# Performance work log

Measured on AMD Instinct MI355X. Metric: run time of the kernel, lower is better.

## Reference

```python
import jax, jax.numpy as jnp
import numpy as np
import math

B, D, H, W, C = 1, 16, 56, 56, 256
WD, WH, WW = 2, 7, 7
NH, NP = 8, 4
N = WD * WH * WW          # 98 tokens per window
HD = C // NH
NWIN = (D // WD) * (H // WH) * (W // WW)  # 512


def layernorm(x, g, b, eps=1e-5):
    m = x.mean(-1, keepdims=True)
    v = jnp.mean((x - m) ** 2, -1, keepdims=True)
    return (x - m) * jax.lax.rsqrt(v + eps) * g + b


def _reference_points():
    zz = (jnp.arange(WD, dtype=jnp.float32) + 0.5) / WD
    yy = (jnp.arange(WH, dtype=jnp.float32) + 0.5) / WH
    xx = (jnp.arange(WW, dtype=jnp.float32) + 0.5) / WW
    gz, gy, gx = jnp.meshgrid(zz, yy, xx, indexing='ij')
    return jnp.stack([gx.ravel(), gy.ravel(), gz.ravel()], -1)  # (N, 3) in xyz order


def _trilinear(value, loc):
    # value: (Bn, N, NH, HD); loc: (Bn, N, NH, NP, 3) normalized xyz in [0,1]
    # grid_sample semantics: align_corners=False, zero padding
    Bn = value.shape[0]
    v = value.transpose(0, 2, 1, 3)  # (Bn, NH, S, HD), S == N (window volume)
    px = loc[..., 0] * WW - 0.5
    py = loc[..., 1] * WH - 0.5
    pz = loc[..., 2] * WD - 0.5
    x0, y0, z0 = jnp.floor(px), jnp.floor(py), jnp.floor(pz)
    out = jnp.zeros(loc.shape[:-1] + (HD,), value.dtype)
    for dz in (0, 1):
        for dy in (0, 1):
            for dx in (0, 1):
                xi, yi, zi = x0 + dx, y0 + dy, z0 + dz
                wgt = (1 - jnp.abs(px - xi)) * (1 - jnp.abs(py - yi)) * (1 - jnp.abs(pz - zi))
                valid = ((xi >= 0) & (xi < WW) & (yi >= 0) & (yi < WH) & (zi >= 0) & (zi < WD)).astype(value.dtype)
                idx = (jnp.clip(zi, 0, WD - 1) * (WH * WW) + jnp.clip(yi, 0, WH - 1) * WW
                       + jnp.clip(xi, 0, WW - 1)).astype(jnp.int32)  # (Bn, N, NH, NP)
                idxf = idx.transpose(0, 2, 1, 3).reshape(Bn, NH, N * NP)
                g = jnp.take_along_axis(v, idxf[..., None], axis=2)  # (Bn, NH, N*NP, HD)
                g = g.reshape(Bn, NH, N, NP, HD).transpose(0, 2, 1, 3, 4)
                out = out + g * (wgt * valid)[..., None]
    return out  # (Bn, N, NH, NP, HD)


def setup_inputs():
    key = jax.random.key(0)
    ks = jax.random.split(key, 12)

    def lin(k, fin, fout):
        s = 1.0 / np.sqrt(fin)
        kw, kb = jax.random.split(k)
        return (jax.random.uniform(kw, (fin, fout), jnp.float32, -s, s),
                jax.random.uniform(kb, (fout,), jnp.float32, -s, s))

    val_w, val_b = lin(ks[2], C, C)
    off_w, off_b = lin(ks[3], C, NH * NP * 3)
    aw_w, aw_b = lin(ks[4], C, NH * NP)
    out_w, out_b = lin(ks[5], C, C)
    proj_w, proj_b = lin(ks[6], C, C)
    fc1_w, fc1_b = lin(ks[7], C, 4 * C)
    fc2_w, fc2_b = lin(ks[8], 4 * C, C)
    return dict(
        x=jax.random.normal(ks[0], (B, D, H, W, C), jnp.float32),
        mask=jax.random.uniform(ks[1], (NWIN, N, WD, WH, WW), jnp.float32),
        norm1_g=jnp.ones((C,), jnp.float32), norm1_b=jnp.zeros((C,), jnp.float32),
        val_w=val_w, val_b=val_b, off_w=off_w, off_b=off_b,
        aw_w=aw_w, aw_b=aw_b, out_w=out_w, out_b=out_b,
        anorm_g=jnp.ones((C,), jnp.float32), anorm_b=jnp.zeros((C,), jnp.float32),
        proj_w=proj_w, proj_b=proj_b,
        norm2_g=jnp.ones((C,), jnp.float32), norm2_b=jnp.zeros((C,), jnp.float32),
        fc1_w=fc1_w, fc1_b=fc1_b, fc2_w=fc2_w, fc2_b=fc2_b)


def reference(x, mask, norm1_g, norm1_b, val_w, val_b, off_w, off_b, aw_w, aw_b,
              out_w, out_b, anorm_g, anorm_b, proj_w, proj_b,
              norm2_g, norm2_b, fc1_w, fc1_b, fc2_w, fc2_b):
    shortcut = x
    xn = layernorm(x, norm1_g, norm1_b)
    # window partition (dims divisible by window, shift_size = 0 -> no pad/roll)
    xw = xn.reshape(B, D // WD, WD, H // WH, WH, W // WW, WW, C)
    xw = xw.transpose(0, 1, 3, 5, 2, 4, 6, 7).reshape(-1, N, C)  # (B*NWIN, N, C)
    Bn = B * NWIN
    # --- PositionEmbeddingSine over the per-window mask ---
    z_e = jnp.cumsum(mask, 2) * mask / math.pi
    y_e = jnp.cumsum(mask, 3) * mask / math.pi
    x_e = jnp.cumsum(mask, 4) * mask / math.pi
    emb = mask * (jnp.sin(x_e) + jnp.sin(math.pi * y_e) + z_e)
    emb = emb.reshape(NWIN, N, N)  # flatten(2); N == WD*WH*WW
    diag = jnp.diagonal(emb, axis1=1, axis2=2)  # (NWIN, N)
    q = (xw.reshape(B, NWIN, N, C) + diag[None, :, :, None]).reshape(Bn, N, C)
    # --- MS3DDeformAttn over single level = window ---
    ref = _reference_points()  # (N, 3)
    value = (xw @ val_w + val_b).reshape(Bn, N, NH, HD)
    off = (q @ off_w + off_b).reshape(Bn, N, NH, NP, 3)
    aw = jax.nn.softmax((q @ aw_w + aw_b).reshape(Bn, N, NH, NP), axis=-1)
    loc = ref[None, :, None, None, :] + off / jnp.array([WW, WH, WD], jnp.float32)
    sampled = _trilinear(value, loc)                       # (Bn, N, NH, NP, HD)
    attn = (sampled * aw[..., None]).sum(3).reshape(Bn, N, C) @ out_w + out_b
    # WindowAttention3D epilogue: proj(norm(x + attn))
    xw = layernorm(xw + attn, anorm_g, anorm_b) @ proj_w + proj_b
    # window reverse
    xr = xw.reshape(B, D // WD, H // WH, W // WW, WD, WH, WW, C)
    xr = xr.transpose(0, 1, 4, 2, 5, 3, 6, 7).reshape(B, D, H, W, C)
    x = shortcut + xr
    # MLP branch
    h = layernorm(x, norm2_g, norm2_b)
    h = jax.nn.gelu(h @ fc1_w + fc1_b)
    return x + (h @ fc2_w + fc2_b)
```

## Files before the change

### kernel.cpp

```cpp
#include <hip/hip_runtime.h>
#include <hip/hip_bf16.h>
#include <hip/hip_fp16.h>

#define B2F(x) __bfloat162float(x)
#define F2B(x) __float2bfloat16(x)

typedef __bf16 bf16x8 __attribute__((ext_vector_type(8)));
typedef float floatx4 __attribute__((ext_vector_type(4)));

static constexpr int MROWS = 50176;
static constexpr int CDIM  = 256;
static constexpr int MCHUNK = 25088;

enum { MODE_BF16 = 0, MODE_VALOFFAW = 1, MODE_REVERSE = 3, MODE_GELU = 4, MODE_FC2 = 5, MODE_ATTN = 6 };

#if defined(__has_builtin)
#if __has_builtin(__builtin_amdgcn_global_load_lds)
#define HAS_GLL 1
#endif
#endif
#ifndef HAS_GLL
#define HAS_GLL 0
#endif


__device__ __forceinline__ void win_decode(int r, int& tok) {
    int w = r / 98, n = r - w * 98;
    int dB = w >> 6, hB = (w >> 3) & 7, wB = w & 7;
    int z = n / 49, n2 = n - z * 49, yy = n2 / 7, xx = n2 - yy * 7;
    tok = ((dB * 2 + z) * 56 + hB * 7 + yy) * 56 + wB * 7 + xx;
}

__device__ __forceinline__ float bf2f(unsigned short u) {
    return __uint_as_float(((unsigned)u) << 16);
}

__device__ __forceinline__ float wave_sum64(float v) {
#pragma unroll
    for (int off = 32; off > 0; off >>= 1) v += __shfl_xor(v, off, 64);
    return v;
}


__global__ __launch_bounds__(256) void fused_pre(
    const float* __restrict__ x, const float* __restrict__ n1g, const float* __restrict__ n1b,
    __hip_bfloat16* __restrict__ xw,
    const float* __restrict__ mask, float* __restrict__ diag, float* __restrict__ csum,
    const float* __restrict__ val_w, const float* __restrict__ off_w,
    const float* __restrict__ aw_w,  const float* __restrict__ out_w,
    const float* __restrict__ proj_w, const float* __restrict__ fc1_w,
    const float* __restrict__ fc2_w,
    __hip_bfloat16* __restrict__ valT, __hip_bfloat16* __restrict__ offawT,
    __hip_bfloat16* __restrict__ outT, __hip_bfloat16* __restrict__ projT,
    __hip_bfloat16* __restrict__ fc1T, __hip_bfloat16* __restrict__ fc2T) {
    const int bid = blockIdx.x;
    const int tid = threadIdx.x;

    if (bid < 2944) {
        const float* src; __hip_bfloat16* dst; int K, N, base;
        if (bid < 256)       { src = val_w;  dst = valT;            K = 256;  N = 256;  base = 0; }
        else if (bid < 352)  { src = off_w;  dst = offawT;          K = 256;  N = 96;   base = 256; }
        else if (bid < 384)  { src = aw_w;   dst = offawT + 96*256; K = 256;  N = 32;   base = 352; }
        else if (bid < 640)  { src = out_w;  dst = outT;            K = 256;  N = 256;  base = 384; }
        else if (bid < 896)  { src = proj_w; dst = projT;           K = 256;  N = 256;  base = 640; }
        else if (bid < 1920) { src = fc1_w;  dst = fc1T;            K = 256;  N = 1024; base = 896; }
        else                 { src = fc2_w;  dst = fc2T;            K = 1024; N = 256;  base = 1920; }
        int i = (bid - base) * 256 + tid;
        if (i >= K * N) return;
        int nn = i / K, kk = i - nn * K;
        dst[(size_t)nn * K + kk] = F2B(src[(size_t)kk * N + nn]);
    } else if (bid < 3140) {
        int r = (bid - 2944) * 256 + tid;
        int n = r % 98;
        int z = n / 49, n2 = n - z * 49, yy = n2 / 7, xx = n2 - yy * 7;
        const float* mb = mask + (size_t)r * 98;
        float m = mb[z * 49 + yy * 7 + xx];
        float sz = 0.f, sy = 0.f, sx = 0.f;
        for (int k = 0; k <= z; ++k)  sz += mb[k * 49 + yy * 7 + xx];
        for (int k = 0; k <= yy; ++k) sy += mb[z * 49 + k * 7 + xx];
        for (int k = 0; k <= xx; ++k) sx += mb[z * 49 + yy * 7 + k];
        const float PI = 3.14159265358979323846f;
        diag[r] = m * (sinf(sx * m / PI) + sinf(sy * m) + sz * m / PI);
    } else if (bid == 3140) {
        if (tid < 96) {
            float s = 0.f;
            for (int k = 0; k < 256; ++k) s += off_w[(size_t)k * 96 + tid];
            csum[tid] = s;
        } else if (tid < 128) {
            int n = tid - 96;
            float s = 0.f;
            for (int k = 0; k < 256; ++k) s += aw_w[(size_t)k * 32 + n];
            csum[tid] = s;
        }
    } else {
        const int lane = tid & 63;
        const int r = (bid - 3141) * 4 + (tid >> 6);
        int tok; win_decode(r, tok);
        const int c0 = lane * 4;
        float4 v = *(const float4*)(x + (size_t)tok * CDIM + c0);
        float mean = wave_sum64(v.x + v.y + v.z + v.w) * (1.f / 256.f);
        float dx = v.x - mean, dy = v.y - mean, dz = v.z - mean, dw = v.w - mean;
        float var = wave_sum64(dx * dx + dy * dy + dz * dz + dw * dw) * (1.f / 256.f);
        float rstd = rsqrtf(var + 1e-5f);
        float4 gg = *(const float4*)(n1g + c0);
        float4 bb = *(const float4*)(n1b + c0);
        __hip_bfloat16 ob[4] = { F2B(dx * rstd * gg.x + bb.x), F2B(dy * rstd * gg.y + bb.y),
                                 F2B(dz * rstd * gg.z + bb.z), F2B(dw * rstd * gg.w + bb.w) };
        *(ushort4*)(xw + (size_t)r * CDIM + c0) = *(const ushort4*)ob;
    }
}


__global__ __launch_bounds__(256) void ln_a_kernel(
    const __hip_bfloat16* __restrict__ s,
    const float* __restrict__ g, const float* __restrict__ b,
    __hip_bfloat16* a2) {
    const int lane = threadIdx.x & 63;
    const int r = blockIdx.x * 4 + (threadIdx.x >> 6);
    const int c0 = lane * 4;
    const size_t base = (size_t)r * CDIM + c0;
    ushort4 sv = *(const ushort4*)(s + base);
    float tx = bf2f(sv.x), ty = bf2f(sv.y), tz = bf2f(sv.z), tw = bf2f(sv.w);
    float mean = wave_sum64(tx + ty + tz + tw) * (1.f / 256.f);
    float dx = tx - mean, dy = ty - mean, dz = tz - mean, dw = tw - mean;
    float var = wave_sum64(dx * dx + dy * dy + dz * dz + dw * dw) * (1.f / 256.f);
    float rstd = rsqrtf(var + 1e-5f);
    float4 gg = *(const float4*)(g + c0);
    float4 bb = *(const float4*)(b + c0);
    __hip_bfloat16 ob[4] = { F2B(dx * rstd * gg.x + bb.x), F2B(dy * rstd * gg.y + bb.y),
                             F2B(dz * rstd * gg.z + bb.z), F2B(dw * rstd * gg.w + bb.w) };
    *(ushort4*)((__hip_bfloat16*)a2 + base) = *(const ushort4*)ob;
}

__global__ __launch_bounds__(256) void ln2_kernel(
    const float* __restrict__ xres,
    const float* __restrict__ g, const float* __restrict__ b,
    __hip_bfloat16* __restrict__ hin) {
    const int lane = threadIdx.x & 63;
    const int r = blockIdx.x * 4 + (threadIdx.x >> 6);
    const int c0 = lane * 4;
    float4 v = *(const float4*)(xres + (size_t)r * CDIM + c0);
    float mean = wave_sum64(v.x + v.y + v.z + v.w) * (1.f / 256.f);
    float dx = v.x - mean, dy = v.y - mean, dz = v.z - mean, dw = v.w - mean;
    float var = wave_sum64(dx * dx + dy * dy + dz * dz + dw * dw) * (1.f / 256.f);
    float rstd = rsqrtf(var + 1e-5f);
    float4 gg = *(const float4*)(g + c0);
    float4 bb = *(const float4*)(b + c0);
    __hip_bfloat16 ob[4] = { F2B(dx * rstd * gg.x + bb.x), F2B(dy * rstd * gg.y + bb.y),
                             F2B(dz * rstd * gg.z + bb.z), F2B(dw * rstd * gg.w + bb.w) };
    *(ushort4*)(hin + (size_t)r * CDIM + c0) = *(const ushort4*)ob;
}


__global__ __launch_bounds__(512, 4) void sample_fused(
    const __half* __restrict__ offaw,
    const __hip_bfloat16* __restrict__ value,
    __hip_bfloat16* __restrict__ ai) {
    __shared__ __align__(16) __hip_bfloat16 vs[98 * 256];
    __shared__ __align__(16) __half os[98 * 128];
    const int tid = threadIdx.x;
    const int w = blockIdx.x;

#if HAS_GLL
    {
        const uint4* vsrc = (const uint4*)(value + (size_t)w * 98 * CDIM);
#pragma unroll
        for (int k = 0; k < 7; ++k) {
            int i = tid + k * 512;
            if (i < 3136)
                __builtin_amdgcn_global_load_lds(
                    (const __attribute__((address_space(1))) void*)(vsrc + i),
                    (__attribute__((address_space(3))) void*)(((uint4*)vs) + i), 16, 0, 0);
        }
        const uint4* osrc = (const uint4*)(offaw + (size_t)w * 98 * 128);
#pragma unroll
        for (int k = 0; k < 4; ++k) {
            int i = tid + k * 512;
            if (i < 1568)
                __builtin_amdgcn_global_load_lds(
                    (const __attribute__((address_space(1))) void*)(osrc + i),
                    (__attribute__((address_space(3))) void*)(((uint4*)os) + i), 16, 0, 0);
        }
    }
#else
    {
        const uint4* vsrc = (const uint4*)(value + (size_t)w * 98 * CDIM);
        uint4* vdst = (uint4*)vs;
        for (int i = tid; i < 3136; i += 512) vdst[i] = vsrc[i];
        const uint4* osrc = (const uint4*)(offaw + (size_t)w * 98 * 128);
        uint4* odst = (uint4*)os;
        for (int i = tid; i < 1568; i += 512) odst[i] = osrc[i];
    }
#endif
    __syncthreads();

    const int lane  = tid & 63;
    const int wave  = tid >> 6;
    const int h     = lane >> 3;
    const int s     = lane & 7;
    const int p     = s >> 1;
    const int jbase = (s & 1) * 4;
    const int boff  = lane * 8;
    const int gbase = lane & ~7;

    for (int r = wave; r < 98; r += 8) {
        int z = r / 49, n2 = r - z * 49, yy = n2 / 7, xx = n2 - yy * 7;
        const __half* orow = os + r * 128;

        float l0 = __half2float(orow[96 + h * 4 + 0]);
        float l1 = __half2float(orow[96 + h * 4 + 1]);
        float l2 = __half2float(orow[96 + h * 4 + 2]);
        float l3 = __half2float(orow[96 + h * 4 + 3]);
        float mx = fmaxf(fmaxf(l0, l1), fmaxf(l2, l3));
        float e0 = __expf(l0 - mx), e1 = __expf(l1 - mx), e2 = __expf(l2 - mx), e3 = __expf(l3 - mx);
        float inv = 1.f / (e0 + e1 + e2 + e3);
        float ep = (p == 0) ? e0 : (p == 1) ? e1 : (p == 2) ? e2 : e3;
        float wp = ep * inv;

        float ox = __half2float(orow[h * 12 + p * 3 + 0]);
        float oy = __half2float(orow[h * 12 + p * 3 + 1]);
        float oz = __half2float(orow[h * 12 + p * 3 + 2]);
        float px = (float)xx + ox, py = (float)yy + oy, pz = (float)z + oz;
        float fx0 = floorf(px), fy0 = floorf(py), fz0 = floorf(pz);
        int ix = (int)fx0, iy = (int)fy0, iz = (int)fz0;
        float fx = px - fx0, fy = py - fy0, fz = pz - fz0;

        uint packed[4];
#pragma unroll
        for (int jj = 0; jj < 4; ++jj) {
            int j = jbase + jj;
            int dzz = j >> 2, dyy = (j >> 1) & 1, dxx = j & 1;
            int zi = iz + dzz, yi = iy + dyy, xi = ix + dxx;
            float wz = dzz ? fz : 1.f - fz;
            float wy = dyy ? fy : 1.f - fy;
            float wxw = dxx ? fx : 1.f - fx;
            bool valid = (zi >= 0) & (zi < 2) & (yi >= 0) & (yi < 7) & (xi >= 0) & (xi < 7);
            float wc = valid ? wp * wz * wy * wxw : 0.f;
            int zc = min(max(zi, 0), 1), yc = min(max(yi, 0), 6), xc = min(max(xi, 0), 6);
            int idx = zc * 49 + yc * 7 + xc;
            packed[jj] = ((uint)(idx * 512) << 16) | (uint)__half_as_ushort(__float2half(wc));
        }

        float a0 = 0.f, a1 = 0.f, a2 = 0.f, a3 = 0.f;
#pragma unroll
        for (int jj = 0; jj < 4; ++jj) {
            uint mine = packed[jj];
#pragma unroll
            for (int sl = 0; sl < 8; ++sl) {
                uint pk = __shfl(mine, gbase + sl, 64);
                float wj = __half2float(__ushort_as_half((unsigned short)(pk & 0xffffu)));
                ushort4 v = *(const ushort4*)((const char*)vs + (pk >> 16) + boff);
                a0 += wj * bf2f(v.x);
                a1 += wj * bf2f(v.y);
                a2 += wj * bf2f(v.z);
                a3 += wj * bf2f(v.w);
            }
        }
        __hip_bfloat16 ob[4] = { F2B(a0), F2B(a1), F2B(a2), F2B(a3) };
        *(ushort4*)(ai + ((size_t)w * 98 + r) * CDIM + lane * 4) = *(const ushort4*)ob;
    }
}


template <int MODE>
__global__ __launch_bounds__(256) void gemm_bt(
    const __hip_bfloat16* __restrict__ A,
    const __hip_bfloat16* __restrict__ Bt,
    const int N, const int K,
    const float* __restrict__ bias0,
    const float* __restrict__ bias1,
    const float* __restrict__ bias2,
    void* C,
    void* extra,
    const void* extra2,
    const float* __restrict__ csum) {
    __shared__ __align__(16) __hip_bfloat16 As[2][128 * 32];
    __shared__ __align__(16) __hip_bfloat16 Bs[2][128 * 32];
    const int tid  = threadIdx.x;
    const int lane = tid & 63;
    const int wave = tid >> 6;
    const int wm = (wave >> 1) * 64;
    const int wn = (wave & 1) * 64;
    const int row0 = blockIdx.x * 128;
    const int col0 = blockIdx.y * 128;
    const int l15 = lane & 15;
    const int quad = lane >> 4;

    floatx4 acc[4][4] = {};

    const int sr = tid >> 2;
    const int sk = (tid & 3) * 8;

    const __hip_bfloat16* Ab = A + (size_t)row0 * K + sr * (size_t)K + sk;
    const __hip_bfloat16* Bb = Bt + (size_t)col0 * K + sr * (size_t)K + sk;
    const size_t half64 = (size_t)64 * K;

    auto stage = [&](int buf, int k0) {
#if HAS_GLL
        __builtin_amdgcn_global_load_lds(
            (const __attribute__((address_space(1))) void*)(Ab + k0),
            (__attribute__((address_space(3))) void*)(&As[buf][sr * 32 + sk]), 16, 0, 0);
        __builtin_amdgcn_global_load_lds(
            (const __attribute__((address_space(1))) void*)(Ab + half64 + k0),
            (__attribute__((address_space(3))) void*)(&As[buf][(sr + 64) * 32 + sk]), 16, 0, 0);
        __builtin_amdgcn_global_load_lds(
            (const __attribute__((address_space(1))) void*)(Bb + k0),
            (__attribute__((address_space(3))) void*)(&Bs[buf][sr * 32 + sk]), 16, 0, 0);
        __builtin_amdgcn_global_load_lds(
            (const __attribute__((address_space(1))) void*)(Bb + half64 + k0),
            (__attribute__((address_space(3))) void*)(&Bs[buf][(sr + 64) * 32 + sk]), 16, 0, 0);
#else
        *reinterpret_cast<uint4*>(&As[buf][sr * 32 + sk]) = *reinterpret_cast<const uint4*>(Ab + k0);
        *reinterpret_cast<uint4*>(&As[buf][(sr + 64) * 32 + sk]) = *reinterpret_cast<const uint4*>(Ab + half64 + k0);
        *reinterpret_cast<uint4*>(&Bs[buf][sr * 32 + sk]) = *reinterpret_cast<const uint4*>(Bb + k0);
        *reinterpret_cast<uint4*>(&Bs[buf][(sr + 64) * 32 + sk]) = *reinterpret_cast<const uint4*>(Bb + half64 + k0);
#endif
    };

    const int nk = K >> 5;
    stage(0, 0);
    for (int t = 0; t < nk; ++t) {
        __syncthreads();
        if (t + 1 < nk) stage((t + 1) & 1, (t + 1) * 32);
        const __hip_bfloat16* Asb = As[t & 1];
        const __hip_bfloat16* Bsb = Bs[t & 1];
        bf16x8 af[4], bfg[4];
#pragma unroll
        for (int i = 0; i < 4; ++i)
            af[i] = *reinterpret_cast<const bf16x8*>(&Asb[(wm + i * 16 + l15) * 32 + quad * 8]);
#pragma unroll
        for (int j = 0; j < 4; ++j)
            bfg[j] = *reinterpret_cast<const bf16x8*>(&Bsb[(wn + j * 16 + l15) * 32 + quad * 8]);
#pragma unroll
        for (int i = 0; i < 4; ++i)
#pragma unroll
            for (int j = 0; j < 4; ++j)
                acc[i][j] = __builtin_amdgcn_mfma_f32_16x16x32_bf16(af[i], bfg[j], acc[i][j], 0, 0, 0);
    }

#pragma unroll
    for (int i = 0; i < 4; ++i) {
#pragma unroll
        for (int j = 0; j < 4; ++j) {
#pragma unroll
            for (int rr = 0; rr < 4; ++rr) {
                int row = row0 + wm + i * 16 + quad * 4 + rr;
                int col = col0 + wn + j * 16 + l15;
                float v = acc[i][j][rr];
                if constexpr (MODE == MODE_BF16) {
                    v += bias0[col];
                    ((__hip_bfloat16*)C)[(size_t)row * N + col] = F2B(v);
                } else if constexpr (MODE == MODE_ATTN) {
                    v += bias0[col];
                    const __hip_bfloat16* xwp = (const __hip_bfloat16*)extra2;
                    v += B2F(xwp[(size_t)row * 256 + col]);
                    ((__hip_bfloat16*)C)[(size_t)row * N + col] = F2B(v);
                } else if constexpr (MODE == MODE_VALOFFAW) {
                    if (col < 256) {
                        v += bias0[col];
                        ((__hip_bfloat16*)C)[(size_t)row * 256 + col] = F2B(v);
                    } else {
                        int c2 = col - 256;
                        const float* diag = (const float*)extra2;
                        v += (c2 < 96 ? bias1[c2] : bias2[c2 - 96]);
                        v += diag[row] * csum[c2];
                        ((__half*)extra)[(size_t)row * 128 + c2] = __float2half(v);
                    }
                } else if constexpr (MODE == MODE_REVERSE) {
                    v += bias0[col];
                    int tok; win_decode(row, tok);
                    const float* xin = (const float*)extra2;
                    ((float*)C)[(size_t)tok * CDIM + col] = xin[(size_t)tok * CDIM + col] + v;
                } else if constexpr (MODE == MODE_GELU) {
                    v += bias0[col];
                    float t2 = 1.5957691216057308f * (v + 0.044715f * v * v * v);
                    v = v / (1.f + __expf(-t2));
                    ((__hip_bfloat16*)C)[(size_t)row * N + col] = F2B(v);
                } else {
                    v += bias0[col];
                    const float* xres = (const float*)extra2;
                    v += xres[(size_t)row * CDIM + col];
                    ((float*)C)[(size_t)row * CDIM + col] = v;
                }
            }
        }
    }
}


extern "C" void kernel_launch(void* const* d_in, const int* in_sizes, int n_in,
                              void* d_out, int out_size, void* d_ws, size_t ws_size,
                              hipStream_t stream) {
    const float* x      = (const float*)d_in[0];
    const float* mask   = (const float*)d_in[1];
    const float* n1g    = (const float*)d_in[2];
    const float* n1b    = (const float*)d_in[3];
    const float* val_w  = (const float*)d_in[4];
    const float* val_b  = (const float*)d_in[5];
    const float* off_w  = (const float*)d_in[6];
    const float* off_b  = (const float*)d_in[7];
    const float* aw_w   = (const float*)d_in[8];
    const float* aw_b   = (const float*)d_in[9];
    const float* out_w  = (const float*)d_in[10];
    const float* out_b  = (const float*)d_in[11];
    const float* ang    = (const float*)d_in[12];
    const float* anb    = (const float*)d_in[13];
    const float* proj_w = (const float*)d_in[14];
    const float* proj_b = (const float*)d_in[15];
    const float* n2g    = (const float*)d_in[16];
    const float* n2b    = (const float*)d_in[17];
    const float* fc1_w  = (const float*)d_in[18];
    const float* fc1_b  = (const float*)d_in[19];
    const float* fc2_w  = (const float*)d_in[20];
    const float* fc2_b  = (const float*)d_in[21];

    char* ws = (char*)d_ws;
    size_t o = 0;
    auto alloc = [&](size_t bytes) {
        size_t r = o;
        o += (bytes + 255) & ~(size_t)255;
        return r;
    };
    const size_t M = MROWS;

    __hip_bfloat16* valT    = (__hip_bfloat16*)(ws + alloc(256 * 256 * 2));
    __hip_bfloat16* offawT  = (__hip_bfloat16*)(ws + alloc(128 * 256 * 2));
    __hip_bfloat16* outT    = (__hip_bfloat16*)(ws + alloc(256 * 256 * 2));
    __hip_bfloat16* projT   = (__hip_bfloat16*)(ws + alloc(256 * 256 * 2));
    __hip_bfloat16* fc1T    = (__hip_bfloat16*)(ws + alloc(1024 * 256 * 2));
    __hip_bfloat16* fc2T    = (__hip_bfloat16*)(ws + alloc(256 * 1024 * 2));
    float*          csum    = (float*)(ws + alloc(128 * 4));
    float*          diag    = (float*)(ws + alloc(M * 4));
    char*           slab1   = ws + alloc(M * 256 * 2);
    char*           region  = ws + o;
    size_t          avail   = (ws_size > o) ? (ws_size - o) : 0;
    (void)in_sizes; (void)n_in; (void)out_size;

    const bool  full = avail >= (size_t)M * 1024 * 2 + 256;
    const int   nch  = full ? 1 : 2;
    const int   MC   = full ? MROWS : MCHUNK;

    __hip_bfloat16* xw    = (__hip_bfloat16*)slab1;
    __hip_bfloat16* a2    = (__hip_bfloat16*)slab1;
    __hip_bfloat16* hin   = (__hip_bfloat16*)slab1;
    __half*         offaw = (__half*)region;
    __hip_bfloat16* ai    = (__hip_bfloat16*)(region + M * 128 * 2);
    __hip_bfloat16* hbuf  = (__hip_bfloat16*)region;
    __hip_bfloat16* value = (__hip_bfloat16*)d_out;
    __hip_bfloat16* attn  = (__hip_bfloat16*)d_out;
    float*          xres  = (float*)d_out;

    dim3 blk(256);
    hipLaunchKernelGGL(fused_pre, dim3(2944 + 196 + 1 + MROWS / 4), blk, 0, stream,
                       x, n1g, n1b, xw, mask, diag, csum,
                       val_w, off_w, aw_w, out_w, proj_w, fc1_w, fc2_w,
                       valT, offawT, outT, projT, fc1T, fc2T);
    hipLaunchKernelGGL((gemm_bt<MODE_VALOFFAW>), dim3(MROWS / 128, 3), blk, 0, stream,
                       xw, valT, 384, 256, val_b, off_b, aw_b,
                       (void*)value, (void*)offaw, (const void*)diag, csum);
    hipLaunchKernelGGL(sample_fused, dim3(MROWS / 98), dim3(512), 0, stream,
                       offaw, value, ai);
    hipLaunchKernelGGL((gemm_bt<MODE_ATTN>), dim3(MROWS / 128, 2), blk, 0, stream,
                       ai, outT, 256, 256, out_b, (const float*)nullptr, (const float*)nullptr,
                       (void*)attn, (void*)nullptr, (const void*)xw, (const float*)nullptr);
    hipLaunchKernelGGL(ln_a_kernel, dim3(MROWS / 4), blk, 0, stream, attn, ang, anb, a2);
    hipLaunchKernelGGL((gemm_bt<MODE_REVERSE>), dim3(MROWS / 128, 2), blk, 0, stream,
                       a2, projT, 256, 256, proj_b, (const float*)nullptr, (const float*)nullptr,
                       (void*)xres, (void*)nullptr, (const void*)x, (const float*)nullptr);
    hipLaunchKernelGGL(ln2_kernel, dim3(MROWS / 4), blk, 0, stream, xres, n2g, n2b, hin);
    for (int c = 0; c < nch; ++c) {
        const __hip_bfloat16* hin_c = hin + (size_t)c * MC * 256;
        float*                out_c = (float*)d_out + (size_t)c * MC * 256;
        hipLaunchKernelGGL((gemm_bt<MODE_GELU>), dim3(MC / 128, 8), blk, 0, stream,
                           hin_c, fc1T, 1024, 256, fc1_b, (const float*)nullptr, (const float*)nullptr,
                           (void*)hbuf, (void*)nullptr, (const void*)nullptr, (const float*)nullptr);
        hipLaunchKernelGGL((gemm_bt<MODE_FC2>), dim3(MC / 128, 2), blk, 0, stream,
                           hbuf, fc2T, 256, 1024, fc2_b, (const float*)nullptr, (const float*)nullptr,
                           (void*)out_c, (void*)nullptr, (const void*)out_c, (const float*)nullptr);
    }
}
```

Measured before the change: 500.2 us.

## Fuse fc1+GELU+fc2 MLP into one kernel keeping hidden activations on-chip

Replaces the separate fc1/GELU GEMM and fc2 GEMM launches, and their chunking logic, with a single fused MLP kernel. Each block of 128 rows keeps its LayerNorm input in LDS, computes 64 hidden columns at a time with MFMA, applies GELU, stages the result in LDS, and accumulates the fc2 product in registers. This removes the round trip of the 50176x1024 bf16 hidden tensor through global memory. In exchange, fc1 and fc2 weight fragments are read straight from global memory without LDS staging. Only 392 blocks are launched, so occupancy and parallelism drop.

```diff
diff --git a/kernel.cpp b/kernel.cpp
--- a/kernel.cpp
+++ b/kernel.cpp
@@ -10,9 +10,8 @@
 
 static constexpr int MROWS = 50176;
 static constexpr int CDIM  = 256;
-static constexpr int MCHUNK = 25088;
-
-enum { MODE_BF16 = 0, MODE_VALOFFAW = 1, MODE_REVERSE = 3, MODE_GELU = 4, MODE_FC2 = 5, MODE_ATTN = 6 };
+
+enum { MODE_BF16 = 0, MODE_VALOFFAW = 1, MODE_REVERSE = 3, MODE_ATTN = 6 };
 
 #if defined(__has_builtin)
 #if __has_builtin(__builtin_amdgcn_global_load_lds)
@@ -371,20 +370,100 @@
                     int tok; win_decode(row, tok);
                     const float* xin = (const float*)extra2;
                     ((float*)C)[(size_t)tok * CDIM + col] = xin[(size_t)tok * CDIM + col] + v;
-                } else if constexpr (MODE == MODE_GELU) {
-                    v += bias0[col];
-                    float t2 = 1.5957691216057308f * (v + 0.044715f * v * v * v);
-                    v = v / (1.f + __expf(-t2));
-                    ((__hip_bfloat16*)C)[(size_t)row * N + col] = F2B(v);
-                } else {
-                    v += bias0[col];
-                    const float* xres = (const float*)extra2;
-                    v += xres[(size_t)row * CDIM + col];
-                    ((float*)C)[(size_t)row * CDIM + col] = v;
                 }
             }
         }
     }
+}
+
+
+__global__ __launch_bounds__(512, 4) void mlp_fused(
+    const __hip_bfloat16* __restrict__ hin,
+    const __hip_bfloat16* __restrict__ fc1T,
+    const __hip_bfloat16* __restrict__ fc2T,
+    const float* __restrict__ fc1_b, const float* __restrict__ fc2_b,
+    float* __restrict__ out) {
+    __shared__ __align__(16) __hip_bfloat16 hs[8 * 128 * 32];
+    __shared__ __align__(16) __hip_bfloat16 as[2 * 128 * 32];
+    const int tid  = threadIdx.x;
+    const int lane = tid & 63;
+    const int w    = tid >> 6;
+    const int r0   = blockIdx.x * 128;
+    const int l15  = lane & 15;
+    const int quad = lane >> 4;
+    const int wm   = (w >> 2) * 64;
+    const int wn   = (w & 3) * 64;
+    const int ac   = (w & 3) * 16;
+
+    {
+        const int row = tid >> 2, ke = (tid & 3) * 8;
+#if HAS_GLL
+#pragma unroll
+        for (int kt = 0; kt < 8; ++kt)
+            __builtin_amdgcn_global_load_lds(
+                (const __attribute__((address_space(1))) void*)(hin + (size_t)(r0 + row) * 256 + kt * 32 + ke),
+                (__attribute__((address_space(3))) void*)(&hs[kt * 4096 + row * 32 + ke]), 16, 0, 0);
+#else
+#pragma unroll
+        for (int kt = 0; kt < 8; ++kt)
+            *(uint4*)(&hs[kt * 4096 + row * 32 + ke]) =
+                *(const uint4*)(hin + (size_t)(r0 + row) * 256 + kt * 32 + ke);
+#endif
+    }
+    floatx4 acc[4][4] = {};
+    const int kt2 = (ac + l15) >> 5, ko = (ac + l15) & 31;
+    __syncthreads();
+
+    for (int kk = 0; kk < 1024; kk += 64) {
+        floatx4 pa[4] = {};
+#pragma unroll
+        for (int ks = 0; ks < 8; ++ks) {
+            bf16x8 b1 = *(const bf16x8*)(fc1T + (size_t)(kk + ac + l15) * 256 + ks * 32 + quad * 8);
+#pragma unroll
+            for (int i = 0; i < 4; ++i) {
+                bf16x8 a = *(const bf16x8*)(&hs[ks * 4096 + (wm + i * 16 + l15) * 32 + quad * 8]);
+                pa[i] = __builtin_amdgcn_mfma_f32_16x16x32_bf16(a, b1, pa[i], 0, 0, 0);
+            }
+        }
+        float bb = fc1_b[kk + ac + l15];
+        __syncthreads();
+#pragma unroll
+        for (int i = 0; i < 4; ++i) {
+#pragma unroll
+            for (int rr = 0; rr < 4; ++rr) {
+                float v = pa[i][rr] + bb;
+                float t2 = 1.5957691216057308f * (v + 0.044715f * v * v * v);
+                v = v / (1.f + __expf(-t2));
+                int row = wm + i * 16 + quad * 4 + rr;
+                as[kt2 * 4096 + row * 32 + ko] = F2B(v);
+            }
+        }
+        __syncthreads();
+#pragma unroll
+        for (int ks = 0; ks < 2; ++ks) {
+            bf16x8 a4[4];
+#pragma unroll
+            for (int i = 0; i < 4; ++i)
+                a4[i] = *(const bf16x8*)(&as[ks * 4096 + (wm + i * 16 + l15) * 32 + quad * 8]);
+#pragma unroll
+            for (int j = 0; j < 4; ++j) {
+                bf16x8 b2 = *(const bf16x8*)(fc2T + (size_t)(wn + j * 16 + l15) * 1024 + kk + ks * 32 + quad * 8);
+#pragma unroll
+                for (int i = 0; i < 4; ++i)
+                    acc[i][j] = __builtin_amdgcn_mfma_f32_16x16x32_bf16(a4[i], b2, acc[i][j], 0, 0, 0);
+            }
+        }
+    }
+#pragma unroll
+    for (int i = 0; i < 4; ++i)
+#pragma unroll
+        for (int j = 0; j < 4; ++j)
+#pragma unroll
+            for (int rr = 0; rr < 4; ++rr) {
+                int row = r0 + wm + i * 16 + quad * 4 + rr;
+                int col = wn + j * 16 + l15;
+                out[(size_t)row * 256 + col] += acc[i][j][rr] + fc2_b[col];
+            }
 }
 
 
@@ -422,6 +501,7 @@
         return r;
     };
     const size_t M = MROWS;
+    const size_t REGION_B = M * 128 * 2 + M * 256 * 2;
 
     __hip_bfloat16* valT    = (__hip_bfloat16*)(ws + alloc(256 * 256 * 2));
     __hip_bfloat16* offawT  = (__hip_bfloat16*)(ws + alloc(128 * 256 * 2));
@@ -432,20 +512,14 @@
     float*          csum    = (float*)(ws + alloc(128 * 4));
     float*          diag    = (float*)(ws + alloc(M * 4));
     char*           slab1   = ws + alloc(M * 256 * 2);
-    char*           region  = ws + o;
-    size_t          avail   = (ws_size > o) ? (ws_size - o) : 0;
-    (void)in_sizes; (void)n_in; (void)out_size;
-
-    const bool  full = avail >= (size_t)M * 1024 * 2 + 256;
-    const int   nch  = full ? 1 : 2;
-    const int   MC   = full ? MROWS : MCHUNK;
+    char*           region  = ws + alloc(REGION_B);
+    (void)ws_size; (void)in_sizes; (void)n_in; (void)out_size;
 
     __hip_bfloat16* xw    = (__hip_bfloat16*)slab1;
     __hip_bfloat16* a2    = (__hip_bfloat16*)slab1;
     __hip_bfloat16* hin   = (__hip_bfloat16*)slab1;
     __half*         offaw = (__half*)region;
     __hip_bfloat16* ai    = (__hip_bfloat16*)(region + M * 128 * 2);
-    __hip_bfloat16* hbuf  = (__hip_bfloat16*)region;
     __hip_bfloat16* value = (__hip_bfloat16*)d_out;
     __hip_bfloat16* attn  = (__hip_bfloat16*)d_out;
     float*          xres  = (float*)d_out;
@@ -468,14 +542,6 @@
                        a2, projT, 256, 256, proj_b, (const float*)nullptr, (const float*)nullptr,
                        (void*)xres, (void*)nullptr, (const void*)x, (const float*)nullptr);
     hipLaunchKernelGGL(ln2_kernel, dim3(MROWS / 4), blk, 0, stream, xres, n2g, n2b, hin);
-    for (int c = 0; c < nch; ++c) {
-        const __hip_bfloat16* hin_c = hin + (size_t)c * MC * 256;
-        float*                out_c = (float*)d_out + (size_t)c * MC * 256;
-        hipLaunchKernelGGL((gemm_bt<MODE_GELU>), dim3(MC / 128, 8), blk, 0, stream,
-                           hin_c, fc1T, 1024, 256, fc1_b, (const float*)nullptr, (const float*)nullptr,
-                           (void*)hbuf, (void*)nullptr, (const void*)nullptr, (const float*)nullptr);
-        hipLaunchKernelGGL((gemm_bt<MODE_FC2>), dim3(MC / 128, 2), blk, 0, stream,
-                           hbuf, fc2T, 256, 1024, fc2_b, (const float*)nullptr, (const float*)nullptr,
-                           (void*)out_c, (void*)nullptr, (const void*)out_c, (const float*)nullptr);
-    }
-}
+    hipLaunchKernelGGL(mlp_fused, dim3(MROWS / 128), dim3(512), 0, stream,
+                       hin, fc1T, fc2T, fc1_b, fc2_b, (float*)d_out);
+}
```

After: 493.0 us. Within noise of the previous version (-1.4%).
